# Kernel tuning notes

Hardware: AMD Instinct MI355X
Metric: run time of the kernel (lower is better)

Reference implementation:

```python
import jax, jax.numpy as jnp
import numpy as np

NUM_NODES = 200000
NUM_EDGES = 640000
RANK = 16
EMBED_DIM = 128


def setup_inputs() -> dict:
    key = jax.random.key(0)
    k1, k2, k3 = jax.random.split(key, 3)
    U = jax.random.normal(k1, (NUM_NODES, RANK), dtype=jnp.float32)
    V = jax.random.normal(k2, (RANK, EMBED_DIM), dtype=jnp.float32)
    edge_index = jax.random.randint(k3, (2, NUM_EDGES), 0, NUM_NODES, dtype=jnp.int64)
    return {"U": U, "V": V, "edge_index": edge_index}


def reference(U, V, edge_index):
    # Low-rank projection: [N, r] @ [r, d] -> [N, d]
    embeddings = jnp.matmul(U, V)
    src, dst = edge_index[0], edge_index[1]
    # Mean aggregation (PyG MessagePassing aggr='mean', source_to_target):
    # gather messages from source nodes, segment-mean into destination nodes.
    msgs = embeddings[src]  # [E, d]
    summed = jax.ops.segment_sum(msgs, dst, num_segments=NUM_NODES)  # [N, d]
    counts = jax.ops.segment_sum(jnp.ones((edge_index.shape[1],), dtype=embeddings.dtype),
                                 dst, num_segments=NUM_NODES)  # [N]
    denom = jnp.maximum(counts, 1.0)  # isolated nodes -> 0 output (scatter-mean semantics)
    return summed / denom[:, None]
```

## Files before the change

kernel.cpp:

```cpp
#include <hip/hip_runtime.h>

#define RANK 16
#define EMBED_DIM 128
#define CAP 32

__global__ __launch_bounds__(256) void fill_slots(
        const int* __restrict__ eiw,
        int* __restrict__ cnt,
        int* __restrict__ ovfcnt,
        int* __restrict__ slots,
        int* __restrict__ ovf,
        int E, int nwords) {
    __shared__ int iflag;
    if (threadIdx.x == 0) iflag = 0;
    __syncthreads();
    {
        int w = 2 * threadIdx.x + 1;
        unsigned int v = (w < nwords) ? ((const unsigned int*)eiw)[w] : 0u;
        if (v) atomicOr(&iflag, 1);
    }
    __syncthreads();
    const bool is32 = (iflag != 0);

    int e = blockIdx.x * 256 + threadIdx.x;
    if (e >= E) return;
    int src, dst;
    if (is32) {
        src = eiw[e];
        dst = eiw[E + e];
    } else {
        src = eiw[2 * e];
        dst = eiw[2 * (E + e)];
    }
    int pos = atomicAdd(&cnt[dst], 1);
    if (pos < CAP) {
        slots[(size_t)dst * CAP + pos] = src;
    } else {
        int o = atomicAdd(ovfcnt, 1);
        ovf[2 * o]     = src;
        ovf[2 * o + 1] = dst;
    }
}

__global__ __launch_bounds__(256) void gather_project(
        const float* __restrict__ U,
        const float* __restrict__ V,
        const int* __restrict__ cnt,
        const int* __restrict__ slots,
        const int* __restrict__ ovfcnt,
        const int* __restrict__ ovf,
        float* __restrict__ out, int N) {
    __shared__ float4 Vs4[RANK * EMBED_DIM / 4];
    __shared__ float accs[32][RANK];
    __shared__ float sinv[32];
    __shared__ int   scnt[32];
    __shared__ int   sslot[32][CAP + 1];

    const int t = threadIdx.x;
    const float4* V4 = (const float4*)V;
    Vs4[t]       = V4[t];
    Vs4[t + 256] = V4[t + 256];

    const int n0 = blockIdx.x * 32;

    if (t < 32) {
        int n = n0 + t;
        int c = (n < N) ? cnt[n] : 0;
        scnt[t] = c;
        sinv[t] = 1.0f / fmaxf((float)c, 1.0f);
    }
    {
        const int4* g4 = (const int4*)(slots + (size_t)n0 * CAP);
        int nd = t >> 3;
        if (n0 + nd < N) {
            int4 v = g4[t];
            sslot[nd][(t & 7) * 4 + 0] = v.x;
            sslot[nd][(t & 7) * 4 + 1] = v.y;
            sslot[nd][(t & 7) * 4 + 2] = v.z;
            sslot[nd][(t & 7) * 4 + 3] = v.w;
        }
    }
    __syncthreads();

    const int g = t >> 4;
    const int j = t & 15;
#pragma unroll
    for (int half = 0; half < 2; ++half) {
        int nd = half * 16 + g;
        int n = n0 + nd;
        float acc = 0.f;
        if (n < N) {
            int deg = scnt[nd];
            int k = deg < CAP ? deg : CAP;
            for (int e = 0; e < k; ++e) {
                int s = sslot[nd][e];
                acc += U[(size_t)s * RANK + j];
            }
            if (deg > CAP) {
                int m = *ovfcnt;
                for (int i = 0; i < m; ++i)
                    if (ovf[2 * i + 1] == n)
                        acc += U[(size_t)ovf[2 * i] * RANK + j];
            }
        }
        accs[nd][j] = acc;
    }
    __syncthreads();

    const int q = t & 31;
    const int w = t >> 5;
#pragma unroll
    for (int r = 0; r < 4; ++r) {
        int nd = 4 * w + r;
        float4 a4 = make_float4(0.f, 0.f, 0.f, 0.f);
#pragma unroll
        for (int k = 0; k < RANK; ++k) {
            float a = accs[nd][k];
            float4 v = Vs4[k * 32 + q];
            a4.x = fmaf(a, v.x, a4.x);
            a4.y = fmaf(a, v.y, a4.y);
            a4.z = fmaf(a, v.z, a4.z);
            a4.w = fmaf(a, v.w, a4.w);
        }
        float s = sinv[nd];
        int n = n0 + nd;
        if (n < N)
            ((float4*)out)[(size_t)n * (EMBED_DIM / 4) + q] =
                make_float4(a4.x * s, a4.y * s, a4.z * s, a4.w * s);
    }
}

extern "C" void kernel_launch(void* const* d_in, const int* in_sizes, int n_in,
                              void* d_out, int out_size, void* d_ws, size_t ws_size,
                              hipStream_t stream) {
    const float* U = (const float*)d_in[0];
    const float* V = (const float*)d_in[1];
    const int* EI = (const int*)d_in[2];
    float* out = (float*)d_out;

    const int N = in_sizes[0] / RANK;
    const int E = in_sizes[2] / 2;
    const int nwords = in_sizes[2];

    int* wsI = (int*)d_ws;
    int* cnt = wsI;
    int* ovfcnt = wsI + N;
    const int slots_off = (N + 1 + 15) & ~15;
    int* slots = wsI + slots_off;
    int* ovf = slots + (size_t)N * CAP;

    hipMemsetAsync(d_ws, 0, (size_t)(N + 1) * sizeof(int), stream);

    fill_slots<<<(E + 255) / 256, 256, 0, stream>>>(
        EI, cnt, ovfcnt, slots, ovf, E, nwords);

    gather_project<<<(N + 31) / 32, 256, 0, stream>>>(
        U, V, cnt, slots, ovfcnt, ovf, out, N);
}
```

Measured before the change: 199.6 us.

## Halve slot capacity, batch four edges per thread, use nontemporal output stores

Slot capacity per destination node drops from 32 to 16. This halves the slot array that gather_project has to read and lets it copy slots into shared memory with plain int4 loads. fill_slots now handles four edges per thread through vectorized int4 index loads, launching a quarter as many blocks. Output rows are written with nontemporal stores so they do not pollute the cache. The trade-off is that high-degree nodes spill to the overflow list more often, and that list is scanned linearly, though the random degree distribution should keep this rare.

```diff
diff --git a/kernel.cpp b/kernel.cpp
--- a/kernel.cpp
+++ b/kernel.cpp
@@ -2,7 +2,9 @@
 
 #define RANK 16
 #define EMBED_DIM 128
-#define CAP 32
+#define CAP 16
+
+typedef float floatx4 __attribute__((ext_vector_type(4)));
 
 __global__ __launch_bounds__(256) void fill_slots(
         const int* __restrict__ eiw,
@@ -22,23 +24,45 @@
     __syncthreads();
     const bool is32 = (iflag != 0);
 
-    int e = blockIdx.x * 256 + threadIdx.x;
-    if (e >= E) return;
-    int src, dst;
-    if (is32) {
-        src = eiw[e];
-        dst = eiw[E + e];
+    const int base = (blockIdx.x * 256 + threadIdx.x) * 4;
+    if (base >= E) return;
+
+    int srcs[4], dsts[4];
+    int ne;
+    if ((E & 3) == 0 && base + 3 < E) {
+        ne = 4;
+        if (is32) {
+            int4 s = *(const int4*)(eiw + base);
+            int4 d = *(const int4*)(eiw + E + base);
+            srcs[0] = s.x; srcs[1] = s.y; srcs[2] = s.z; srcs[3] = s.w;
+            dsts[0] = d.x; dsts[1] = d.y; dsts[2] = d.z; dsts[3] = d.w;
+        } else {
+            const int4* p = (const int4*)(eiw + 2 * base);
+            const int4* q = (const int4*)(eiw + 2 * (E + base));
+            int4 v0 = p[0], v1 = p[1], d0 = q[0], d1 = q[1];
+            srcs[0] = v0.x; srcs[1] = v0.z; srcs[2] = v1.x; srcs[3] = v1.z;
+            dsts[0] = d0.x; dsts[1] = d0.z; dsts[2] = d1.x; dsts[3] = d1.z;
+        }
     } else {
-        src = eiw[2 * e];
-        dst = eiw[2 * (E + e)];
+        ne = 0;
+        for (int e = base; e < E && e < base + 4; ++e, ++ne) {
+            srcs[ne] = is32 ? eiw[e] : eiw[2 * e];
+            dsts[ne] = is32 ? eiw[E + e] : eiw[2 * (E + e)];
+        }
     }
-    int pos = atomicAdd(&cnt[dst], 1);
-    if (pos < CAP) {
-        slots[(size_t)dst * CAP + pos] = src;
-    } else {
-        int o = atomicAdd(ovfcnt, 1);
-        ovf[2 * o]     = src;
-        ovf[2 * o + 1] = dst;
+
+#pragma unroll
+    for (int j = 0; j < 4; ++j) {
+        if (j >= ne) break;
+        int dst = dsts[j];
+        int pos = atomicAdd(&cnt[dst], 1);
+        if (pos < CAP) {
+            slots[(size_t)dst * CAP + pos] = srcs[j];
+        } else {
+            int o = atomicAdd(ovfcnt, 1);
+            ovf[2 * o]     = srcs[j];
+            ovf[2 * o + 1] = dst;
+        }
     }
 }
 
@@ -54,7 +78,7 @@
     __shared__ float accs[32][RANK];
     __shared__ float sinv[32];
     __shared__ int   scnt[32];
-    __shared__ int   sslot[32][CAP + 1];
+    __shared__ int4  sslot4[32 * CAP / 4];
 
     const int t = threadIdx.x;
     const float4* V4 = (const float4*)V;
@@ -69,19 +93,13 @@
         scnt[t] = c;
         sinv[t] = 1.0f / fmaxf((float)c, 1.0f);
     }
-    {
+    if (t < 128) {
         const int4* g4 = (const int4*)(slots + (size_t)n0 * CAP);
-        int nd = t >> 3;
-        if (n0 + nd < N) {
-            int4 v = g4[t];
-            sslot[nd][(t & 7) * 4 + 0] = v.x;
-            sslot[nd][(t & 7) * 4 + 1] = v.y;
-            sslot[nd][(t & 7) * 4 + 2] = v.z;
-            sslot[nd][(t & 7) * 4 + 3] = v.w;
-        }
+        if (n0 + (t >> 2) < N) sslot4[t] = g4[t];
     }
     __syncthreads();
 
+    const int* sslot = (const int*)sslot4;
     const int g = t >> 4;
     const int j = t & 15;
 #pragma unroll
@@ -93,7 +111,7 @@
             int deg = scnt[nd];
             int k = deg < CAP ? deg : CAP;
             for (int e = 0; e < k; ++e) {
-                int s = sslot[nd][e];
+                int s = sslot[nd * CAP + e];
                 acc += U[(size_t)s * RANK + j];
             }
             if (deg > CAP) {
@@ -124,9 +142,12 @@
         }
         float s = sinv[nd];
         int n = n0 + nd;
-        if (n < N)
-            ((float4*)out)[(size_t)n * (EMBED_DIM / 4) + q] =
-                make_float4(a4.x * s, a4.y * s, a4.z * s, a4.w * s);
+        if (n < N) {
+            floatx4 o;
+            o.x = a4.x * s; o.y = a4.y * s; o.z = a4.z * s; o.w = a4.w * s;
+            __builtin_nontemporal_store(
+                o, (floatx4*)out + (size_t)n * (EMBED_DIM / 4) + q);
+        }
     }
 }
 
@@ -151,7 +172,7 @@
 
     hipMemsetAsync(d_ws, 0, (size_t)(N + 1) * sizeof(int), stream);
 
-    fill_slots<<<(E + 255) / 256, 256, 0, stream>>>(
+    fill_slots<<<(E + 1023) / 1024, 256, 0, stream>>>(
         EI, cnt, ovfcnt, slots, ovf, E, nwords);
 
     gather_project<<<(N + 31) / 32, 256, 0, stream>>>(
```

New measurement: 187.7 us. 6.0% less time.
